# Optimization experiments

Measured on AMD Instinct MI355X. Metric: run time of the kernel, lower is better.

## Reference

```python
import jax, jax.numpy as jnp
import numpy as np

B, S, DIM, H, D = 4, 2048, 1024, 16, 64
WINDOW = 512  # max_mem_segments * window_size


def _rotary_angles(seq_len, dim_head):
    inv_freq = 1.0 / (10000.0 ** (jnp.arange(0, dim_head, 2, dtype=jnp.float32) / dim_head))
    freqs = jnp.arange(seq_len, dtype=jnp.float32)[:, None] * inv_freq[None, :]  # [S, D/2]
    return jnp.repeat(freqs, 2, axis=-1)  # [S, D] interleaved


def _rotate_half(x):
    x1 = x[..., 0::2]
    x2 = x[..., 1::2]
    return jnp.stack((-x2, x1), axis=-1).reshape(x.shape)


def _apply_rotary(x, angles):
    # x: [b h n d], angles: [n d]
    return x * jnp.cos(angles) + _rotate_half(x) * jnp.sin(angles)


def setup_inputs() -> dict:
    key = jax.random.key(0)
    ks = jax.random.split(key, 7)
    tokens = jax.random.normal(ks[0], (B, S, DIM), dtype=jnp.float32)
    value_residual = jax.random.normal(ks[1], (B, H, S, D), dtype=jnp.float32)
    s = 0.02
    Wq = jax.random.normal(ks[2], (DIM, H * D), dtype=jnp.float32) * s
    Wkv = jax.random.normal(ks[3], (DIM, 2 * H * D), dtype=jnp.float32) * s
    Wout = jax.random.normal(ks[4], (H * D, DIM), dtype=jnp.float32) * s
    Wgate = jax.random.normal(ks[5], (DIM, H), dtype=jnp.float32) * s
    Wmix = jax.random.normal(ks[6], (DIM, H), dtype=jnp.float32) * s
    return {"tokens": tokens, "value_residual": value_residual, "Wq": Wq,
            "Wkv": Wkv, "Wout": Wout, "Wgate": Wgate, "Wmix": Wmix}


def reference(tokens, value_residual, Wq, Wkv, Wout, Wgate, Wmix):
    b, n, dim = tokens.shape
    scale = D ** -0.5

    def split_heads(t):  # [b n (h d)] -> [b h n d]
        return t.reshape(b, n, H, D).transpose(0, 2, 1, 3)

    q = split_heads(tokens @ Wq)
    kv = tokens @ Wkv
    k = split_heads(kv[..., : H * D])
    v = split_heads(kv[..., H * D:])

    q = q * scale

    # value-residual lerp: v.lerp(value_residual, mix)
    mix = jax.nn.sigmoid(jnp.einsum('bnd,dh->bhn', tokens, Wmix))[..., None]  # [b h n 1]
    v = v + (value_residual - v) * mix

    angles = _rotary_angles(n, D)
    q = _apply_rotary(q, angles)
    k = _apply_rotary(k, angles)

    sim = jnp.einsum('bhid,bhjd->bhij', q, k)

    # fixed-window causal mask: dist = i - j; masked if dist < 0 or dist > WINDOW
    pos = jnp.arange(n)
    dist = pos[:, None] - pos[None, :]
    mask = (dist < 0) | (dist > WINDOW)
    neg = -jnp.finfo(sim.dtype).max
    sim = jnp.where(mask[None, None], neg, sim)

    attn = jax.nn.softmax(sim, axis=-1)
    out = jnp.einsum('bhij,bhjd->bhid', attn, v)

    gates = jax.nn.sigmoid(jnp.einsum('bnd,dh->bhn', tokens, Wgate))[..., None]  # [b h n 1]
    out = out * gates

    out = out.transpose(0, 2, 1, 3).reshape(b, n, H * D)
    return out @ Wout
```

## Files before the change

### kernel.cpp

```cpp
#include <hip/hip_runtime.h>

#define NH 16
#define SLEN 2048
#define DMODEL 1024
#define DHEAD 64
#define WIN 512
#define NB 4

typedef unsigned short u16;
typedef unsigned int u32;
typedef unsigned long long u64;
typedef __attribute__((ext_vector_type(8))) __bf16 bf16x8;
typedef __attribute__((ext_vector_type(4))) float floatx4;

__device__ __forceinline__ float b2f(u32 bits16) {
  union { u32 i; float f; } x; x.i = bits16 << 16; return x.f;
}
__device__ __forceinline__ u16 f2b(float f) {
  union { float f; u32 i; } x; x.f = f;
  u32 r = x.i + 0x7fffu + ((x.i >> 16) & 1u);
  return (u16)(r >> 16);
}

__device__ __forceinline__ void gl2lds16(const u16* g, u16* l) {
  __builtin_amdgcn_global_load_lds(
      (const __attribute__((address_space(1))) unsigned int*)g,
      (__attribute__((address_space(3))) unsigned int*)l, 16, 0, 0);
}

template<int OFF>
__device__ __forceinline__ bf16x8 ldsr128(u32 addr) {
  bf16x8 r;
  if constexpr (OFF == 0)
    asm volatile("ds_read_b128 %0, %1" : "=v"(r) : "v"(addr));
  else
    asm volatile("ds_read_b128 %0, %1 offset:%2" : "=v"(r) : "v"(addr), "i"(OFF));
  return r;
}

#define WAIT_VM6   asm volatile("s_waitcnt vmcnt(6)" ::: "memory")
#define WAIT_VM0   asm volatile("s_waitcnt vmcnt(0)" ::: "memory")
#define WAIT_LGKM8 asm volatile("s_waitcnt lgkmcnt(8)" ::: "memory")
#define WAIT_LGKM0 asm volatile("s_waitcnt lgkmcnt(0)" ::: "memory")

__global__ __launch_bounds__(256) void prep_all(
    const float* __restrict__ tokens, const float* __restrict__ Wq,
    const float* __restrict__ Wkv, const float* __restrict__ Wout,
    const float* __restrict__ Wmix, const float* __restrict__ Wgate,
    u64* __restrict__ tokA64, u16* __restrict__ WqkvT, u16* __restrict__ WoutT,
    u16* __restrict__ Wmg, float2* __restrict__ rtab) {
  __shared__ u16 T[64][72];
  const int blk = blockIdx.x, tid = threadIdx.x;
  if (blk < 8192) {
    int i = blk * 256 + tid;
    float4 f = reinterpret_cast<const float4*>(tokens)[i];
    union { u16 u[4]; u64 ll; } pk;
    pk.u[0] = f2b(f.x); pk.u[1] = f2b(f.y); pk.u[2] = f2b(f.z); pk.u[3] = f2b(f.w);
    tokA64[i] = pk.ll;
  } else if (blk < 9216) {
    const float* src; u16* dst; int ld, nb, n0, k0;
    if (blk < 8960) {
      int tile = blk - 8192;
      n0 = (tile % 48) * 64; k0 = (tile / 48) * 64;
      if (n0 < 1024) { src = Wq; ld = 1024; nb = n0; }
      else { src = Wkv; ld = 2048; nb = n0 - 1024; }
      dst = WqkvT;
    } else {
      int tile = blk - 8960;
      n0 = (tile % 16) * 64; k0 = (tile / 16) * 64;
      src = Wout; ld = 1024; nb = n0; dst = WoutT;
    }
#pragma unroll
    for (int i = 0; i < 16; ++i) {
      int e = i * 256 + tid;
      int kr = e >> 6, nc = e & 63;
      T[kr][nc] = f2b(src[(size_t)(k0 + kr) * ld + nb + nc]);
    }
    __syncthreads();
#pragma unroll
    for (int i = 0; i < 16; ++i) {
      int e = i * 256 + tid;
      int nr = e >> 6, kc = e & 63;
      dst[(size_t)(n0 + nr) * 1024 + k0 + kc] = T[kc][nr];
    }
  } else if (blk < 9344) {
    int idx = (blk - 9216) * 256 + tid;
    int n = idx >> 10, k = idx & 1023;
    float v = (n < 16) ? Wmix[k * 16 + n] : Wgate[k * 16 + (n - 16)];
    Wmg[idx] = f2b(v);
  } else {
    int idx = (blk - 9344) * 256 + tid;
    int s = idx >> 5, t = idx & 31;
    float inv = __expf((float)t * -0.2878231366f);
    float ang = (float)s * inv;
    float sn, cs;
    __sincosf(ang, &sn, &cs);
    rtab[idx] = make_float2(cs, sn);
  }
}

__global__ __launch_bounds__(256) void mixgate_mfma(const u16* __restrict__ A,
    const u16* __restrict__ Wmg, float* __restrict__ mixws, float* __restrict__ gatews) {
  const int lane = threadIdx.x & 63, w = threadIdx.x >> 6;
  const int lm = lane & 15, quad = lane >> 4;
  const int row0 = (blockIdx.x * 4 + w) * 32;

  floatx4 acc[2][2];
#pragma unroll
  for (int i = 0; i < 2; ++i)
#pragma unroll
    for (int j = 0; j < 2; ++j)
      acc[i][j] = (floatx4){0.f, 0.f, 0.f, 0.f};

#pragma unroll 4
  for (int k0 = 0; k0 < 1024; k0 += 32) {
    bf16x8 af[2], bf[2];
#pragma unroll
    for (int mt = 0; mt < 2; ++mt)
      af[mt] = *reinterpret_cast<const bf16x8*>(
          &A[(size_t)(row0 + mt * 16 + lm) * 1024 + k0 + quad * 8]);
#pragma unroll
    for (int nt = 0; nt < 2; ++nt)
      bf[nt] = *reinterpret_cast<const bf16x8*>(
          &Wmg[(size_t)(nt * 16 + lm) * 1024 + k0 + quad * 8]);
#pragma unroll
    for (int mt = 0; mt < 2; ++mt)
#pragma unroll
      for (int nt = 0; nt < 2; ++nt)
        acc[mt][nt] = __builtin_amdgcn_mfma_f32_16x16x32_bf16(af[mt], bf[nt], acc[mt][nt], 0, 0, 0);
  }

#pragma unroll
  for (int mt = 0; mt < 2; ++mt)
#pragma unroll
    for (int r = 0; r < 4; ++r) {
      int grow = row0 + mt * 16 + quad * 4 + r;
      int b = grow >> 11, s = grow & 2047;
#pragma unroll
      for (int nt = 0; nt < 2; ++nt) {
        int n = nt * 16 + lm;
        float sig = 1.0f / (1.0f + __expf(-acc[mt][nt][r]));
        int h = n & 15;
        (n < 16 ? mixws : gatews)[(b * NH + h) * SLEN + s] = sig;
      }
    }
}

template<int MODE>
__global__ __launch_bounds__(512, 2) void gemm_pipe(
    const u16* __restrict__ A, const u16* __restrict__ Bt,
    float* __restrict__ C,
    u16* __restrict__ qws, u16* __restrict__ kws, u16* __restrict__ vws,
    const float* __restrict__ vres, const float* __restrict__ mixws,
    const float2* __restrict__ rtab, int N) {
  __shared__ u16 smem[73728];
  const int tid = threadIdx.x;
  const int nbx = N >> 7;
  const int wg = (blockIdx.x & 7) * (gridDim.x >> 3) + (blockIdx.x >> 3);
  const int bx = wg % nbx, by = wg / nbx;
  const int row0 = by * 256, col0 = bx * 128;
  const int w = tid >> 6, lane = tid & 63;
  const int wr = (w >> 1) * 64, wc = (w & 1) * 64;
  const int lm = lane & 15, quad = lane >> 4;
  const int NT = 16;
  const int sr = tid >> 3, sc = tid & 7;
  const int sl0 = (sr * 8 + sc) * 8;
  const u16* gA = A + (size_t)(row0 + sr) * 1024 + ((sc ^ (sr & 7)) << 3);
  const u16* gB = Bt + (size_t)(col0 + sr) * 1024 + ((sc ^ (sr & 7)) << 3);

  const u32 ldsbase = (u32)(size_t)(__attribute__((address_space(3))) u16*)smem;
  u32 arow[2], brow[2];
#pragma unroll
  for (int j = 0; j < 2; ++j) {
    u32 cslot = (u32)((j * 4 + quad) ^ (lm & 7));
    arow[j] = (u32)(wr + lm) * 128 + cslot * 16;
    brow[j] = (u32)(wc + lm) * 128 + cslot * 16;
  }

  floatx4 acc[4][4];
#pragma unroll
  for (int i = 0; i < 4; ++i)
#pragma unroll
    for (int j = 0; j < 4; ++j)
      acc[i][j] = (floatx4){0.f, 0.f, 0.f, 0.f};

  auto stage3 = [&](u16* Sa, u16* Sb, int ks, int half) {
    if (half == 0) {
      gl2lds16(gA + ks, Sa + sl0);
      gl2lds16(gA + 65536 + ks, Sa + 4096 + sl0);
      gl2lds16(gB + ks, Sb + sl0);
    } else {
      gl2lds16(gA + 131072 + ks, Sa + 8192 + sl0);
      gl2lds16(gA + 196608 + ks, Sa + 12288 + sl0);
      gl2lds16(gB + 65536 + ks, Sb + 4096 + sl0);
    }
  };

#pragma unroll
  for (int tt = 0; tt < 2; ++tt) {
    u16* Sa = smem + tt * 24576;
    u16* Sb = Sa + 16384;
    stage3(Sa, Sb, tt * 64, 0);
    stage3(Sa, Sb, tt * 64, 1);
  }

  int cur = 0;
  for (int t = 0; t < NT; ++t) {
    int sidx = cur + 2; if (sidx >= 3) sidx -= 3;
    u16* Sa = smem + sidx * 24576;
    u16* Sb = Sa + 16384;
    const int ks = (t + 2) << 6;
    const bool do_stage = t < NT - 2;
    const u32 abase = ldsbase + (u32)cur * 49152u;

    if (t < NT - 1) { WAIT_VM6; } else { WAIT_VM0; }
    __builtin_amdgcn_s_barrier();

    const u32 a0 = abase + arow[0], b0 = abase + 32768u + brow[0];
    const u32 a1 = abase + arow[1], b1 = abase + 32768u + brow[1];
    bf16x8 af0[4], bf0[4], af1[4], bf1[4];
    af0[0] = ldsr128<0>(a0);    af0[1] = ldsr128<2048>(a0);
    af0[2] = ldsr128<4096>(a0); af0[3] = ldsr128<6144>(a0);
    bf0[0] = ldsr128<0>(b0);    bf0[1] = ldsr128<2048>(b0);
    bf0[2] = ldsr128<4096>(b0); bf0[3] = ldsr128<6144>(b0);
    af1[0] = ldsr128<0>(a1);    af1[1] = ldsr128<2048>(a1);
    af1[2] = ldsr128<4096>(a1); af1[3] = ldsr128<6144>(a1);
    bf1[0] = ldsr128<0>(b1);    bf1[1] = ldsr128<2048>(b1);
    bf1[2] = ldsr128<4096>(b1); bf1[3] = ldsr128<6144>(b1);
    if (do_stage) { stage3(Sa, Sb, ks, 0); stage3(Sa, Sb, ks, 1); }
    __builtin_amdgcn_sched_barrier(0);
    WAIT_LGKM8;
    __builtin_amdgcn_sched_barrier(0);
    __builtin_amdgcn_s_setprio(1);
#pragma unroll
    for (int mt = 0; mt < 4; ++mt)
#pragma unroll
      for (int nt = 0; nt < 4; ++nt)
        acc[mt][nt] = __builtin_amdgcn_mfma_f32_16x16x32_bf16(
            af0[mt], bf0[nt], acc[mt][nt], 0, 0, 0);
    __builtin_amdgcn_s_setprio(0);
    WAIT_LGKM0;
    __builtin_amdgcn_sched_barrier(0);
    __builtin_amdgcn_s_setprio(1);
#pragma unroll
    for (int mt = 0; mt < 4; ++mt)
#pragma unroll
      for (int nt = 0; nt < 4; ++nt)
        acc[mt][nt] = __builtin_amdgcn_mfma_f32_16x16x32_bf16(
            af1[mt], bf1[nt], acc[mt][nt], 0, 0, 0);
    __builtin_amdgcn_s_setprio(0);

    cur += 1; if (cur >= 3) cur -= 3;
  }

  if (MODE == 0) {
#pragma unroll
    for (int mt = 0; mt < 4; ++mt)
#pragma unroll
      for (int r = 0; r < 4; ++r) {
        int grow = row0 + wr + mt * 16 + quad * 4 + r;
#pragma unroll
        for (int nt = 0; nt < 4; ++nt)
          C[(size_t)grow * N + col0 + wc + nt * 16 + lm] = acc[mt][nt][r];
      }
  } else {
    const int seg = col0 >> 10;
    if (seg < 2) {
      u16* dst = seg ? kws : qws;
      const float qs = seg ? 1.0f : 0.125f;
      const int colb = (col0 & 1023) + wc;
#pragma unroll
      for (int mt = 0; mt < 4; ++mt)
#pragma unroll
        for (int r = 0; r < 4; ++r) {
          int sg = row0 + wr + mt * 16 + quad * 4 + r;
          int b = sg >> 11, s = sg & 2047;
#pragma unroll
          for (int nt = 0; nt < 4; ++nt) {
            int nn = colb + nt * 16 + lm;
            int h = nn >> 6, d = nn & 63;
            float val = acc[mt][nt][r] * qs;
            float2 cs = rtab[(s << 5) + (d >> 1)];
            float partner = __shfl_xor(val, 1);
            float o = (d & 1) ? fmaf(val, cs.x, partner * cs.y)
                              : fmaf(val, cs.x, -partner * cs.y);
            dst[((size_t)((b * NH + h) * SLEN + s)) * 64 + d] = f2b(o);
          }
        }
    } else {
      const int h0 = (col0 - 2048) >> 6;
      const int p = (w & 1);
      const int b = row0 >> 11, s0 = row0 & 2047;
      const int bh = b * NH + h0 + p;
      u16 (*Vt)[264] = reinterpret_cast<u16(*)[264]>(smem + p * 16896);
      __syncthreads();
#pragma unroll
      for (int mt = 0; mt < 4; ++mt)
#pragma unroll
        for (int nt = 0; nt < 4; ++nt) {
          const int d = nt * 16 + lm;
          const int sl = wr + mt * 16 + quad * 4;
          union { u16 u[4]; u64 ll; } pk;
#pragma unroll
          for (int r = 0; r < 4; ++r) {
            int s = s0 + sl + r;
            float val = acc[mt][nt][r];
            float mv = mixws[bh * SLEN + s];
            float o = val + (vres[((size_t)(bh * SLEN + s)) * 64 + d] - val) * mv;
            pk.u[r] = f2b(o);
          }
          *reinterpret_cast<u64*>(&Vt[d][sl]) = pk.ll;
        }
      __syncthreads();
#pragma unroll
      for (int it = 0; it < 8; ++it) {
        int idx = it * 512 + tid;
        int ph = idx >> 11, rem = idx & 2047;
        int d = rem >> 5, ch = rem & 31;
        const u16* src = smem + ph * 16896 + d * 264 + ch * 8;
        u16* dst = vws + ((size_t)((b * NH + h0 + ph) * 64 + d)) * SLEN + s0 + ch * 8;
        *reinterpret_cast<uint4*>(dst) = *reinterpret_cast<const uint4*>(src);
      }
    }
  }
}

__global__ __launch_bounds__(256) void attn_mfma_kernel(
    const u16* __restrict__ q, const u16* __restrict__ k, const u16* __restrict__ vt,
    const float* __restrict__ gate, u16* __restrict__ X) {
  __shared__ __align__(16) u16 Ks[2][4096];
  __shared__ __align__(16) u16 Vs[2][4096];
  __shared__ __align__(16) u16 Ps[4][16][72];
  const int tid = threadIdx.x;
  const int w = tid >> 6, lane = tid & 63;
  const int lm = lane & 15, quad = lane >> 4;
  const int blk = blockIdx.x;
  const int qt = blk & 31;
  const int h = (blk >> 5) & 15;
  const int b = blk >> 9;
  const int bh = b * NH + h;
  const int q0 = qt * 64;
  const size_t kqbase = (size_t)bh * SLEN * 64;
  const size_t vbase  = (size_t)bh * 64 * SLEN;

  bf16x8 qf[2];
  {
    const u16* qrow = q + kqbase + (size_t)(q0 + w * 16 + lm) * 64;
    qf[0] = *reinterpret_cast<const bf16x8*>(qrow + quad * 8);
    qf[1] = *reinterpret_cast<const bf16x8*>(qrow + 32 + quad * 8);
  }

  floatx4 o[4];
#pragma unroll
  for (int nt = 0; nt < 4; ++nt) o[nt] = (floatx4){0.f, 0.f, 0.f, 0.f};
  float lsum = 0.f;
  const int iq = q0 + w * 16 + lm;

  const int c_first = (q0 >= WIN) ? ((q0 - WIN) >> 6) : 0;
  const int c_last = q0 >> 6;

  const int sr = tid >> 3;
  const int scz = ((tid & 7) ^ (sr & 7)) * 8;
  const u32 ksbase = (u32)(size_t)(__attribute__((address_space(3))) u16*)&Ks[0][0];
  const u32 vsbase = (u32)(size_t)(__attribute__((address_space(3))) u16*)&Vs[0][0];
  const u32 psbase = (u32)(size_t)(__attribute__((address_space(3))) u16*)&Ps[0][0][0];
  const int rxa8 = lm & 7;
  const u32 rowoff = (u32)lm * 128 + (u32)((quad ^ rxa8) * 16);
  const u32 paddr = psbase + (u32)(w * 16 + lm) * 144 + (u32)quad * 16;

  auto stage = [&](int c, int buf) {
    const u16* kg = k + kqbase + (size_t)(c << 6) * 64;
    const u16* vg = vt + vbase + (c << 6);
    u16* Kd = &Ks[buf][0]; u16* Vd = &Vs[buf][0];
    gl2lds16(kg + sr * 64 + scz, Kd + tid * 8);
    gl2lds16(kg + (sr + 32) * 64 + scz, Kd + 2048 + tid * 8);
    gl2lds16(vg + (size_t)sr * SLEN + scz, Vd + tid * 8);
    gl2lds16(vg + (size_t)(sr + 32) * SLEN + scz, Vd + 2048 + tid * 8);
  };

  stage(c_first, 0);
  int cur = 0;
  for (int c = c_first; c <= c_last; ++c) {
    const int c0 = c << 6;
    __syncthreads();
    if (c < c_last) stage(c + 1, cur ^ 1);

    const u32 kof = ksbase + (u32)(cur << 13) + rowoff;
    const u32 kof4 = kof ^ 64u;
    bf16x8 k00 = ldsr128<0>(kof),     k01 = ldsr128<2048>(kof),
           k02 = ldsr128<4096>(kof),  k03 = ldsr128<6144>(kof);
    bf16x8 k10 = ldsr128<0>(kof4),    k11 = ldsr128<2048>(kof4),
           k12 = ldsr128<4096>(kof4), k13 = ldsr128<6144>(kof4);
    __builtin_amdgcn_sched_barrier(0);
    WAIT_LGKM0;
    __builtin_amdgcn_sched_barrier(0);
    floatx4 st[4];
    const floatx4 z4 = (floatx4){0.f, 0.f, 0.f, 0.f};
    __builtin_amdgcn_s_setprio(1);
    st[0] = __builtin_amdgcn_mfma_f32_16x16x32_bf16(k00, qf[0], z4, 0, 0, 0);
    st[0] = __builtin_amdgcn_mfma_f32_16x16x32_bf16(k10, qf[1], st[0], 0, 0, 0);
    st[1] = __builtin_amdgcn_mfma_f32_16x16x32_bf16(k01, qf[0], z4, 0, 0, 0);
    st[1] = __builtin_amdgcn_mfma_f32_16x16x32_bf16(k11, qf[1], st[1], 0, 0, 0);
    st[2] = __builtin_amdgcn_mfma_f32_16x16x32_bf16(k02, qf[0], z4, 0, 0, 0);
    st[2] = __builtin_amdgcn_mfma_f32_16x16x32_bf16(k12, qf[1], st[2], 0, 0, 0);
    st[3] = __builtin_amdgcn_mfma_f32_16x16x32_bf16(k03, qf[0], z4, 0, 0, 0);
    st[3] = __builtin_amdgcn_mfma_f32_16x16x32_bf16(k13, qf[1], st[3], 0, 0, 0);
    __builtin_amdgcn_s_setprio(0);

    const bool need_mask = (c == c_first && q0 >= WIN) || (c == c_last);
    if (need_mask) {
#pragma unroll
      for (int mt = 0; mt < 4; ++mt)
#pragma unroll
        for (int r = 0; r < 4; ++r) {
          int j = c0 + mt * 16 + quad * 4 + r;
          bool valid = (j <= iq) && (j >= iq - WIN);
          if (!valid) st[mt][r] = -3.0e38f;
        }
    }
    float p[4][4], psum = 0.f;
#pragma unroll
    for (int mt = 0; mt < 4; ++mt)
#pragma unroll
      for (int r = 0; r < 4; ++r) {
        p[mt][r] = __expf(st[mt][r]);
        psum += p[mt][r];
      }
    psum += __shfl_xor(psum, 16);
    psum += __shfl_xor(psum, 32);
    lsum += psum;
#pragma unroll
    for (int mt = 0; mt < 4; ++mt) {
      union { u16 u[4]; u64 ll; } pk;
#pragma unroll
      for (int r = 0; r < 4; ++r) pk.u[r] = f2b(p[mt][r]);
      *reinterpret_cast<u64*>(&Ps[w][lm][mt * 16 + quad * 4]) = pk.ll;
    }
    __builtin_amdgcn_wave_barrier();
    __builtin_amdgcn_s_waitcnt(0xC07F);
    __builtin_amdgcn_wave_barrier();

    bf16x8 pa0 = ldsr128<0>(paddr), pa1 = ldsr128<64>(paddr);
    const u32 vof = vsbase + (u32)(cur << 13) + rowoff;
    const u32 vof4 = vof ^ 64u;
    bf16x8 v00 = ldsr128<0>(vof),     v01 = ldsr128<2048>(vof),
           v02 = ldsr128<4096>(vof),  v03 = ldsr128<6144>(vof);
    bf16x8 v10 = ldsr128<0>(vof4),    v11 = ldsr128<2048>(vof4),
           v12 = ldsr128<4096>(vof4), v13 = ldsr128<6144>(vof4);
    __builtin_amdgcn_sched_barrier(0);
    WAIT_LGKM0;
    __builtin_amdgcn_sched_barrier(0);
    __builtin_amdgcn_s_setprio(1);
    o[0] = __builtin_amdgcn_mfma_f32_16x16x32_bf16(pa0, v00, o[0], 0, 0, 0);
    o[0] = __builtin_amdgcn_mfma_f32_16x16x32_bf16(pa1, v10, o[0], 0, 0, 0);
    o[1] = __builtin_amdgcn_mfma_f32_16x16x32_bf16(pa0, v01, o[1], 0, 0, 0);
    o[1] = __builtin_amdgcn_mfma_f32_16x16x32_bf16(pa1, v11, o[1], 0, 0, 0);
    o[2] = __builtin_amdgcn_mfma_f32_16x16x32_bf16(pa0, v02, o[2], 0, 0, 0);
    o[2] = __builtin_amdgcn_mfma_f32_16x16x32_bf16(pa1, v12, o[2], 0, 0, 0);
    o[3] = __builtin_amdgcn_mfma_f32_16x16x32_bf16(pa0, v03, o[3], 0, 0, 0);
    o[3] = __builtin_amdgcn_mfma_f32_16x16x32_bf16(pa1, v13, o[3], 0, 0, 0);
    __builtin_amdgcn_s_setprio(0);

    cur ^= 1;
  }
  float linv[4], g[4];
#pragma unroll
  for (int r = 0; r < 4; ++r) {
    linv[r] = 1.0f / __shfl(lsum, quad * 4 + r);
    g[r] = gate[bh * SLEN + q0 + w * 16 + quad * 4 + r];
  }
#pragma unroll
  for (int r = 0; r < 4; ++r) {
    int i = q0 + w * 16 + quad * 4 + r;
    u16* xrow = X + ((size_t)(b * SLEN + i)) * 1024 + h * 64;
#pragma unroll
    for (int nt = 0; nt < 4; ++nt)
      xrow[nt * 16 + lm] = f2b(o[nt][r] * linv[r] * g[r]);
  }
}

extern "C" void kernel_launch(void* const* d_in, const int* in_sizes, int n_in,
                              void* d_out, int out_size, void* d_ws, size_t ws_size,
                              hipStream_t stream) {
  (void)in_sizes; (void)n_in; (void)out_size; (void)ws_size;
  const float* tokens = (const float*)d_in[0];
  const float* vres   = (const float*)d_in[1];
  const float* Wq     = (const float*)d_in[2];
  const float* Wkv    = (const float*)d_in[3];
  const float* Wout   = (const float*)d_in[4];
  const float* Wgate  = (const float*)d_in[5];
  const float* Wmix   = (const float*)d_in[6];
  float* out = (float*)d_out;

  char* p = (char*)d_ws;
  auto alloc = [&](size_t bytes) { char* r = p; p += (bytes + 255) & ~(size_t)255; return r; };
  u16*  tokA   = (u16*)alloc(8192ull * 1024 * 2);
  u16*  WqkvT  = (u16*)alloc(3072ull * 1024 * 2);
  u16*  WoutT  = (u16*)alloc(1024ull * 1024 * 2);
  u16*  Wmg    = (u16*)alloc(32ull * 1024 * 2);
  float2* rtab = (float2*)alloc(65536ull * 8);
  u16*  qws    = (u16*)alloc(8388608ull * 2);
  u16*  kws    = (u16*)alloc(8388608ull * 2);
  u16*  vws    = (u16*)alloc(8388608ull * 2);
  u16*  Xws    = (u16*)alloc(8388608ull * 2);
  float* mixws = (float*)alloc(131072ull * 4);
  float* gatews= (float*)alloc(131072ull * 4);

  prep_all<<<9600, 256, 0, stream>>>(tokens, Wq, Wkv, Wout, Wmix, Wgate,
      (u64*)tokA, WqkvT, WoutT, Wmg, rtab);
  mixgate_mfma<<<64, 256, 0, stream>>>(tokA, Wmg, mixws, gatews);
  gemm_pipe<1><<<768, 512, 0, stream>>>(tokA, WqkvT, nullptr,
      qws, kws, vws, vres, mixws, rtab, 3072);
  attn_mfma_kernel<<<2048, 256, 0, stream>>>(qws, kws, vws, gatews, Xws);
  gemm_pipe<0><<<256, 512, 0, stream>>>(Xws, WoutT, out,
      nullptr, nullptr, nullptr, nullptr, nullptr, nullptr, 1024);
}
```

Measured before the change: 273.7 us.

## Enlarge GEMM tiles to 256x256 with double-buffered, quarter-split LDS pipeline

```diff
diff --git a/kernel.cpp b/kernel.cpp
--- a/kernel.cpp
+++ b/kernel.cpp
@@ -38,10 +38,11 @@
   return r;
 }
 
-#define WAIT_VM6   asm volatile("s_waitcnt vmcnt(6)" ::: "memory")
+#define WAIT_VM8   asm volatile("s_waitcnt vmcnt(8)" ::: "memory")
 #define WAIT_VM0   asm volatile("s_waitcnt vmcnt(0)" ::: "memory")
-#define WAIT_LGKM8 asm volatile("s_waitcnt lgkmcnt(8)" ::: "memory")
 #define WAIT_LGKM0 asm volatile("s_waitcnt lgkmcnt(0)" ::: "memory")
+#define SCHEDB     __builtin_amdgcn_sched_barrier(0)
+#define SBAR       __builtin_amdgcn_s_barrier()
 
 __global__ __launch_bounds__(256) void prep_all(
     const float* __restrict__ tokens, const float* __restrict__ Wq,
@@ -153,127 +154,156 @@
     u16* __restrict__ qws, u16* __restrict__ kws, u16* __restrict__ vws,
     const float* __restrict__ vres, const float* __restrict__ mixws,
     const float2* __restrict__ rtab, int N) {
-  __shared__ u16 smem[73728];
+  __shared__ u16 smem[65536];
   const int tid = threadIdx.x;
-  const int nbx = N >> 7;
+  const int nbx = N >> 8;
   const int wg = (blockIdx.x & 7) * (gridDim.x >> 3) + (blockIdx.x >> 3);
   const int bx = wg % nbx, by = wg / nbx;
-  const int row0 = by * 256, col0 = bx * 128;
+  const int row0 = by * 256, col0 = bx * 256;
   const int w = tid >> 6, lane = tid & 63;
-  const int wr = (w >> 1) * 64, wc = (w & 1) * 64;
+  const int wm = w >> 2, wn = w & 3;
   const int lm = lane & 15, quad = lane >> 4;
   const int NT = 16;
+
   const int sr = tid >> 3, sc = tid & 7;
-  const int sl0 = (sr * 8 + sc) * 8;
-  const u16* gA = A + (size_t)(row0 + sr) * 1024 + ((sc ^ (sr & 7)) << 3);
-  const u16* gB = Bt + (size_t)(col0 + sr) * 1024 + ((sc ^ (sr & 7)) << 3);
-
-  const u32 ldsbase = (u32)(size_t)(__attribute__((address_space(3))) u16*)smem;
-  u32 arow[2], brow[2];
-#pragma unroll
-  for (int j = 0; j < 2; ++j) {
-    u32 cslot = (u32)((j * 4 + quad) ^ (lm & 7));
-    arow[j] = (u32)(wr + lm) * 128 + cslot * 16;
-    brow[j] = (u32)(wc + lm) * 128 + cslot * 16;
-  }
-
-  floatx4 acc[4][4];
-#pragma unroll
-  for (int i = 0; i < 4; ++i)
+  const u16* gA0 = A + (size_t)(row0 + sr) * 1024 + ((sc ^ (sr & 7)) << 3);
+  const u16* gB0 = Bt + (size_t)(col0 + sr) * 1024 + ((sc ^ (sr & 7)) << 3);
+
+  const u32 ldsb = (u32)(size_t)(__attribute__((address_space(3))) u16*)smem;
+  const u32 xorq = (u32)(quad ^ (lm & 7)) * 16;
+  const u32 aR = (u32)(wm * 128 + lm) * 128 + xorq;
+  const u32 bR = 32768u + (u32)(wn * 64 + lm) * 128 + xorq;
+
+  floatx4 acc[8][4];
+#pragma unroll
+  for (int i = 0; i < 8; ++i)
 #pragma unroll
     for (int j = 0; j < 4; ++j)
       acc[i][j] = (floatx4){0.f, 0.f, 0.f, 0.f};
 
-  auto stage3 = [&](u16* Sa, u16* Sb, int ks, int half) {
-    if (half == 0) {
-      gl2lds16(gA + ks, Sa + sl0);
-      gl2lds16(gA + 65536 + ks, Sa + 4096 + sl0);
-      gl2lds16(gB + ks, Sb + sl0);
-    } else {
-      gl2lds16(gA + 131072 + ks, Sa + 8192 + sl0);
-      gl2lds16(gA + 196608 + ks, Sa + 12288 + sl0);
-      gl2lds16(gB + 65536 + ks, Sb + 4096 + sl0);
-    }
+  auto stageA2 = [&](int buf, int t2, int h) {
+    const u16* g = gA0 + (size_t)h * 131072 + t2 * 64;
+    u16* d = smem + buf * 32768 + h * 8192 + (tid << 3);
+    gl2lds16(g, d);
+    gl2lds16(g + 65536, d + 4096);
   };
-
-#pragma unroll
-  for (int tt = 0; tt < 2; ++tt) {
-    u16* Sa = smem + tt * 24576;
-    u16* Sb = Sa + 16384;
-    stage3(Sa, Sb, tt * 64, 0);
-    stage3(Sa, Sb, tt * 64, 1);
-  }
-
-  int cur = 0;
+  auto stageB2 = [&](int buf, int t2, int h) {
+    const u16* g = gB0 + (size_t)h * 131072 + t2 * 64;
+    u16* d = smem + buf * 32768 + 16384 + h * 8192 + (tid << 3);
+    gl2lds16(g, d);
+    gl2lds16(g + 65536, d + 4096);
+  };
+
+  stageA2(0, 0, 0); stageA2(0, 0, 1); stageB2(0, 0, 0); stageB2(0, 0, 1);
+  stageA2(1, 1, 0); stageA2(1, 1, 1); stageB2(1, 1, 0); stageB2(1, 1, 1);
+
   for (int t = 0; t < NT; ++t) {
-    int sidx = cur + 2; if (sidx >= 3) sidx -= 3;
-    u16* Sa = smem + sidx * 24576;
-    u16* Sb = Sa + 16384;
-    const int ks = (t + 2) << 6;
-    const bool do_stage = t < NT - 2;
-    const u32 abase = ldsbase + (u32)cur * 49152u;
-
-    if (t < NT - 1) { WAIT_VM6; } else { WAIT_VM0; }
-    __builtin_amdgcn_s_barrier();
-
-    const u32 a0 = abase + arow[0], b0 = abase + 32768u + brow[0];
-    const u32 a1 = abase + arow[1], b1 = abase + 32768u + brow[1];
-    bf16x8 af0[4], bf0[4], af1[4], bf1[4];
-    af0[0] = ldsr128<0>(a0);    af0[1] = ldsr128<2048>(a0);
-    af0[2] = ldsr128<4096>(a0); af0[3] = ldsr128<6144>(a0);
-    bf0[0] = ldsr128<0>(b0);    bf0[1] = ldsr128<2048>(b0);
-    bf0[2] = ldsr128<4096>(b0); bf0[3] = ldsr128<6144>(b0);
-    af1[0] = ldsr128<0>(a1);    af1[1] = ldsr128<2048>(a1);
-    af1[2] = ldsr128<4096>(a1); af1[3] = ldsr128<6144>(a1);
-    bf1[0] = ldsr128<0>(b1);    bf1[1] = ldsr128<2048>(b1);
-    bf1[2] = ldsr128<4096>(b1); bf1[3] = ldsr128<6144>(b1);
-    if (do_stage) { stage3(Sa, Sb, ks, 0); stage3(Sa, Sb, ks, 1); }
-    __builtin_amdgcn_sched_barrier(0);
-    WAIT_LGKM8;
-    __builtin_amdgcn_sched_barrier(0);
+    const int cur = t & 1;
+    const u32 base = ldsb + (u32)cur * 65536u;
+    const bool ds = t < NT - 2;
+
+    if (t < NT - 1) { WAIT_VM8; } else { WAIT_VM0; }
+    SBAR;
+
+    bf16x8 a0[4], a1[4], b00[2], b10[2], b01[2], b11[2];
+    {
+      u32 aa = base + aR;
+      a0[0] = ldsr128<0>(aa);    a0[1] = ldsr128<2048>(aa);
+      a0[2] = ldsr128<4096>(aa); a0[3] = ldsr128<6144>(aa);
+      u32 ab = aa ^ 64u;
+      a1[0] = ldsr128<0>(ab);    a1[1] = ldsr128<2048>(ab);
+      a1[2] = ldsr128<4096>(ab); a1[3] = ldsr128<6144>(ab);
+      u32 ba = base + bR;
+      b00[0] = ldsr128<0>(ba);   b00[1] = ldsr128<2048>(ba);
+      u32 bb = ba ^ 64u;
+      b10[0] = ldsr128<0>(bb);   b10[1] = ldsr128<2048>(bb);
+    }
+    SCHEDB; SBAR; WAIT_LGKM0; SCHEDB;
     __builtin_amdgcn_s_setprio(1);
 #pragma unroll
-    for (int mt = 0; mt < 4; ++mt)
-#pragma unroll
-      for (int nt = 0; nt < 4; ++nt)
-        acc[mt][nt] = __builtin_amdgcn_mfma_f32_16x16x32_bf16(
-            af0[mt], bf0[nt], acc[mt][nt], 0, 0, 0);
+    for (int i = 0; i < 4; ++i)
+#pragma unroll
+      for (int j = 0; j < 2; ++j) {
+        acc[i][j] = __builtin_amdgcn_mfma_f32_16x16x32_bf16(a0[i], b00[j], acc[i][j], 0, 0, 0);
+        acc[i][j] = __builtin_amdgcn_mfma_f32_16x16x32_bf16(a1[i], b10[j], acc[i][j], 0, 0, 0);
+      }
     __builtin_amdgcn_s_setprio(0);
-    WAIT_LGKM0;
-    __builtin_amdgcn_sched_barrier(0);
+    SBAR;
+
+    {
+      u32 ba = base + bR + 4096u;
+      b01[0] = ldsr128<0>(ba);   b01[1] = ldsr128<2048>(ba);
+      u32 bb = ba ^ 64u;
+      b11[0] = ldsr128<0>(bb);   b11[1] = ldsr128<2048>(bb);
+    }
+    SCHEDB; SBAR; WAIT_LGKM0; SCHEDB;
     __builtin_amdgcn_s_setprio(1);
 #pragma unroll
-    for (int mt = 0; mt < 4; ++mt)
-#pragma unroll
-      for (int nt = 0; nt < 4; ++nt)
-        acc[mt][nt] = __builtin_amdgcn_mfma_f32_16x16x32_bf16(
-            af1[mt], bf1[nt], acc[mt][nt], 0, 0, 0);
+    for (int i = 0; i < 4; ++i)
+#pragma unroll
+      for (int j = 0; j < 2; ++j) {
+        acc[i][2 + j] = __builtin_amdgcn_mfma_f32_16x16x32_bf16(a0[i], b01[j], acc[i][2 + j], 0, 0, 0);
+        acc[i][2 + j] = __builtin_amdgcn_mfma_f32_16x16x32_bf16(a1[i], b11[j], acc[i][2 + j], 0, 0, 0);
+      }
     __builtin_amdgcn_s_setprio(0);
-
-    cur += 1; if (cur >= 3) cur -= 3;
+    SBAR;
+
+    {
+      u32 aa = base + aR + 8192u;
+      a0[0] = ldsr128<0>(aa);    a0[1] = ldsr128<2048>(aa);
+      a0[2] = ldsr128<4096>(aa); a0[3] = ldsr128<6144>(aa);
+      u32 ab = aa ^ 64u;
+      a1[0] = ldsr128<0>(ab);    a1[1] = ldsr128<2048>(ab);
+      a1[2] = ldsr128<4096>(ab); a1[3] = ldsr128<6144>(ab);
+    }
+    if (ds) { stageB2(cur, t + 2, 0); stageB2(cur, t + 2, 1); }
+    SCHEDB; SBAR; WAIT_LGKM0; SCHEDB;
+    __builtin_amdgcn_s_setprio(1);
+#pragma unroll
+    for (int i = 0; i < 4; ++i)
+#pragma unroll
+      for (int j = 0; j < 2; ++j) {
+        acc[4 + i][j] = __builtin_amdgcn_mfma_f32_16x16x32_bf16(a0[i], b00[j], acc[4 + i][j], 0, 0, 0);
+        acc[4 + i][j] = __builtin_amdgcn_mfma_f32_16x16x32_bf16(a1[i], b10[j], acc[4 + i][j], 0, 0, 0);
+      }
+    __builtin_amdgcn_s_setprio(0);
+    SBAR;
+
+    if (ds) { stageA2(cur, t + 2, 0); stageA2(cur, t + 2, 1); }
+    SCHEDB; SBAR; SCHEDB;
+    __builtin_amdgcn_s_setprio(1);
+#pragma unroll
+    for (int i = 0; i < 4; ++i)
+#pragma unroll
+      for (int j = 0; j < 2; ++j) {
+        acc[4 + i][2 + j] = __builtin_amdgcn_mfma_f32_16x16x32_bf16(a0[i], b01[j], acc[4 + i][2 + j], 0, 0, 0);
+        acc[4 + i][2 + j] = __builtin_amdgcn_mfma_f32_16x16x32_bf16(a1[i], b11[j], acc[4 + i][2 + j], 0, 0, 0);
+      }
+    __builtin_amdgcn_s_setprio(0);
+    SBAR;
   }
 
   if (MODE == 0) {
 #pragma unroll
-    for (int mt = 0; mt < 4; ++mt)
+    for (int mt = 0; mt < 8; ++mt)
 #pragma unroll
       for (int r = 0; r < 4; ++r) {
-        int grow = row0 + wr + mt * 16 + quad * 4 + r;
+        int grow = row0 + wm * 128 + mt * 16 + quad * 4 + r;
 #pragma unroll
         for (int nt = 0; nt < 4; ++nt)
-          C[(size_t)grow * N + col0 + wc + nt * 16 + lm] = acc[mt][nt][r];
+          C[(size_t)grow * N + col0 + wn * 64 + nt * 16 + lm] = acc[mt][nt][r];
       }
   } else {
     const int seg = col0 >> 10;
     if (seg < 2) {
       u16* dst = seg ? kws : qws;
       const float qs = seg ? 1.0f : 0.125f;
-      const int colb = (col0 & 1023) + wc;
-#pragma unroll
-      for (int mt = 0; mt < 4; ++mt)
+      const int colb = (col0 & 1023) + wn * 64;
+#pragma unroll
+      for (int mt = 0; mt < 8; ++mt)
 #pragma unroll
         for (int r = 0; r < 4; ++r) {
-          int sg = row0 + wr + mt * 16 + quad * 4 + r;
+          int sg = row0 + wm * 128 + mt * 16 + quad * 4 + r;
           int b = sg >> 11, s = sg & 2047;
 #pragma unroll
           for (int nt = 0; nt < 4; ++nt) {
@@ -289,17 +319,16 @@
         }
     } else {
       const int h0 = (col0 - 2048) >> 6;
-      const int p = (w & 1);
       const int b = row0 >> 11, s0 = row0 & 2047;
-      const int bh = b * NH + h0 + p;
-      u16 (*Vt)[264] = reinterpret_cast<u16(*)[264]>(smem + p * 16896);
+      const int bh = b * NH + h0 + wn;
+      u16* VtW = smem + wn * 16384;
       __syncthreads();
 #pragma unroll
-      for (int mt = 0; mt < 4; ++mt)
+      for (int mt = 0; mt < 8; ++mt)
 #pragma unroll
         for (int nt = 0; nt < 4; ++nt) {
           const int d = nt * 16 + lm;
-          const int sl = wr + mt * 16 + quad * 4;
+          const int sl = wm * 128 + mt * 16 + quad * 4;
           union { u16 u[4]; u64 ll; } pk;
 #pragma unroll
           for (int r = 0; r < 4; ++r) {
@@ -309,17 +338,17 @@
             float o = val + (vres[((size_t)(bh * SLEN + s)) * 64 + d] - val) * mv;
             pk.u[r] = f2b(o);
           }
-          *reinterpret_cast<u64*>(&Vt[d][sl]) = pk.ll;
+          *reinterpret_cast<u64*>(&VtW[d * 256 + sl]) = pk.ll;
         }
       __syncthreads();
 #pragma unroll
-      for (int it = 0; it < 8; ++it) {
+      for (int it = 0; it < 16; ++it) {
         int idx = it * 512 + tid;
-        int ph = idx >> 11, rem = idx & 2047;
+        int hd = idx >> 11, rem = idx & 2047;
         int d = rem >> 5, ch = rem & 31;
-        const u16* src = smem + ph * 16896 + d * 264 + ch * 8;
-        u16* dst = vws + ((size_t)((b * NH + h0 + ph) * 64 + d)) * SLEN + s0 + ch * 8;
-        *reinterpret_cast<uint4*>(dst) = *reinterpret_cast<const uint4*>(src);
+        const u16* src = smem + hd * 16384 + d * 256 + ch * 8;
+        u16* dstp = vws + ((size_t)((b * NH + h0 + hd) * 64 + d)) * SLEN + s0 + ch * 8;
+        *reinterpret_cast<uint4*>(dstp) = *reinterpret_cast<const uint4*>(src);
       }
     }
   }
@@ -391,9 +420,9 @@
            k02 = ldsr128<4096>(kof),  k03 = ldsr128<6144>(kof);
     bf16x8 k10 = ldsr128<0>(kof4),    k11 = ldsr128<2048>(kof4),
            k12 = ldsr128<4096>(kof4), k13 = ldsr128<6144>(kof4);
-    __builtin_amdgcn_sched_barrier(0);
+    SCHEDB;
     WAIT_LGKM0;
-    __builtin_amdgcn_sched_barrier(0);
+    SCHEDB;
     floatx4 st[4];
     const floatx4 z4 = (floatx4){0.f, 0.f, 0.f, 0.f};
     __builtin_amdgcn_s_setprio(1);
@@ -447,9 +476,9 @@
            v02 = ldsr128<4096>(vof),  v03 = ldsr128<6144>(vof);
     bf16x8 v10 = ldsr128<0>(vof4),    v11 = ldsr128<2048>(vof4),
            v12 = ldsr128<4096>(vof4), v13 = ldsr128<6144>(vof4);
-    __builtin_amdgcn_sched_barrier(0);
+    SCHEDB;
     WAIT_LGKM0;
-    __builtin_amdgcn_sched_barrier(0);
+    SCHEDB;
     __builtin_amdgcn_s_setprio(1);
     o[0] = __builtin_amdgcn_mfma_f32_16x16x32_bf16(pa0, v00, o[0], 0, 0, 0);
     o[0] = __builtin_amdgcn_mfma_f32_16x16x32_bf16(pa1, v10, o[0], 0, 0, 0);
@@ -509,9 +538,9 @@
   prep_all<<<9600, 256, 0, stream>>>(tokens, Wq, Wkv, Wout, Wmix, Wgate,
       (u64*)tokA, WqkvT, WoutT, Wmg, rtab);
   mixgate_mfma<<<64, 256, 0, stream>>>(tokA, Wmg, mixws, gatews);
-  gemm_pipe<1><<<768, 512, 0, stream>>>(tokA, WqkvT, nullptr,
+  gemm_pipe<1><<<384, 512, 0, stream>>>(tokA, WqkvT, nullptr,
       qws, kws, vws, vres, mixws, rtab, 3072);
   attn_mfma_kernel<<<2048, 256, 0, stream>>>(qws, kws, vws, gatews, Xws);
-  gemm_pipe<0><<<256, 512, 0, stream>>>(Xws, WoutT, out,
+  gemm_pipe<0><<<128, 512, 0, stream>>>(Xws, WoutT, out,
       nullptr, nullptr, nullptr, nullptr, nullptr, nullptr, 1024);
 }
```

Measured after the change: 296.3 us. 1.08x slower.
